# Kernel tuning notes

Hardware: AMD Instinct MI355X
Metric: run time of the kernel (lower is better)

Reference implementation:

```python
import jax, jax.numpy as jnp
import numpy as np

NUM_HEADS = 4
SPLIT_SIZE = 8  # idx == 1 -> H_sp = H, W_sp = split_size (vertical stripe windows)


def setup_inputs() -> dict:
    key = jax.random.key(0)
    k1, k2, k3 = jax.random.split(key, 3)
    temp = jax.random.normal(k1, (16, 3, 128, 64, 64), dtype=jnp.float32)
    conv_w = jax.random.normal(k2, (128, 1, 3, 3), dtype=jnp.float32) * 0.1  # depthwise LePE conv
    conv_b = jax.random.normal(k3, (128,), dtype=jnp.float32) * 0.1
    return {"temp": temp, "conv_w": conv_w, "conv_b": conv_b}


def reference(temp, conv_w, conv_b):
    B, _, C, H, W = temp.shape
    H_sp, W_sp = H, SPLIT_SIZE          # idx == 1 cross-shaped window
    # H % H_sp == 0 and W % W_sp == 0 -> F.pad amounts are zero here
    nH, nW = H // H_sp, W // W_sp
    L = H_sp * W_sp                     # tokens per window
    hd = C // NUM_HEADS
    scale = hd ** -0.5

    q, k, v = temp[:, 0], temp[:, 1], temp[:, 2]  # each [B, C, H, W]

    def im2cswin(x):
        # img2windows: B C H W -> (B*nH*nW, L, C) then split heads -> (Bw, nh, L, hd)
        x = x.reshape(B, C, nH, H_sp, nW, W_sp).transpose(0, 2, 4, 3, 5, 1)
        x = x.reshape(-1, L, NUM_HEADS, hd).transpose(0, 2, 1, 3)
        return x

    qw = im2cswin(q) * scale            # (Bw, nh, L, hd)
    kw = im2cswin(k)

    # get_rpe: window-partition v as images, depthwise 3x3 conv for LePE
    vimg = v.reshape(B, C, nH, H_sp, nW, W_sp).transpose(0, 2, 4, 1, 3, 5)
    vimg = vimg.reshape(-1, C, H_sp, W_sp)  # (Bw, C, H_sp, W_sp)
    rpe = jax.lax.conv_general_dilated(
        vimg, conv_w, window_strides=(1, 1), padding="SAME",
        dimension_numbers=("NCHW", "OIHW", "NCHW"), feature_group_count=C,
    ) + conv_b[None, :, None, None]
    rpe = rpe.reshape(-1, NUM_HEADS, hd, L).transpose(0, 1, 3, 2)  # (Bw, nh, L, hd)
    vw = vimg.reshape(-1, NUM_HEADS, hd, L).transpose(0, 1, 3, 2)

    attn = jax.nn.softmax(jnp.einsum("wnld,wnmd->wnlm", qw, kw), axis=-1)
    out = jnp.einsum("wnlm,wnmd->wnld", attn, vw) + rpe  # (Bw, nh, L, hd)

    out = out.transpose(0, 2, 1, 3).reshape(-1, L, C)    # (Bw, L, C)
    # windows2img: (Bw, L, C) -> (B, H, W, C)
    out = out.reshape(B, nH, nW, H_sp, W_sp, C).transpose(0, 1, 3, 2, 4, 5)
    out = out.reshape(B, H, W, C)
    return out.reshape(B, H * W, C)
```

## Files before the change

kernel.cpp:

```cpp
#include <hip/hip_runtime.h>

typedef __attribute__((ext_vector_type(8))) short short8;
typedef __attribute__((ext_vector_type(4))) short short4_t;
typedef __attribute__((ext_vector_type(4))) float float4_t;
typedef __attribute__((ext_vector_type(4))) int int4_t;

#define CH_STRIDE 4096
#define IMG_STRIDE 524288
#define HW 4096
#define V520 520

static __device__ __forceinline__ short f2b(float x) {
    unsigned u = __builtin_bit_cast(unsigned, x);
    u = (u + 0x7fffu + ((u >> 16) & 1u)) >> 16;
    return (short)u;
}
static __device__ __forceinline__ float bitsf(unsigned u) { return __builtin_bit_cast(float, u); }
static __device__ __forceinline__ unsigned bitsu(float f) { return __builtin_bit_cast(unsigned, f); }

__global__ __launch_bounds__(512) void cswin_fused(
    const float* __restrict__ temp, const float* __restrict__ cw,
    const float* __restrict__ cb, float* __restrict__ out)
{
    __shared__ short Kc[64 * 40];
    __shared__ short Vt[32 * V520];

    int bx = blockIdx.x;
    int nw = bx >> 6;
    int r  = bx & 63;
    int b  = r >> 2;
    int n  = r & 3;

    int t    = threadIdx.x;
    int wv   = t >> 6;
    int lane = t & 63;
    int mr   = lane & 15;
    int q    = lane >> 4;

    const float* tq = temp + (size_t)b * 3 * IMG_STRIDE + (size_t)(n * 32) * CH_STRIDE + nw * 8;
    const float* tk = tq + IMG_STRIDE;
    const float* tv = tk + IMG_STRIDE;

    int row0 = wv * 64;
    const float qscale = 0.2550348889072310f;

    short8 Qf[4];
    #pragma unroll
    for (int qt = 0; qt < 4; ++qt) {
        int l = row0 + qt * 16 + mr;
        int sp = (l >> 3) * 64 + (l & 7);
        short8 f;
        #pragma unroll
        for (int j = 0; j < 8; ++j)
            f[j] = f2b(tq[(q * 8 + j) * CH_STRIDE + sp] * qscale);
        Qf[qt] = f;
    }

    float4_t zero4 = {0.f, 0.f, 0.f, 0.f};
    float4_t acc[2][4];
    #pragma unroll
    for (int dt = 0; dt < 2; ++dt)
        #pragma unroll
        for (int qt = 0; qt < 4; ++qt)
            acc[dt][qt] = zero4;
    float lsum[4] = {0.f, 0.f, 0.f, 0.f};

    int ld  = t >> 4;
    int seg = t & 15;
    const float* tkld = tk + (size_t)ld * CH_STRIDE;
    const float* tvld = tv + (size_t)ld * CH_STRIDE;

    int lb0 = seg * 4;
    int sp0 = (lb0 >> 3) * 64 + (lb0 & 7);
    float4_t k4 = *reinterpret_cast<const float4_t*>(tkld + sp0);
    float4_t v4 = *reinterpret_cast<const float4_t*>(tvld + sp0);

    int s0lane = (q & 1) * 32 + mr;
    int s1lane = s0lane + 16;
    bool hiq = (q >= 2);

    for (int ch = 0; ch < 8; ++ch) {
        __syncthreads();
        {
            int kl = seg * 4;
            Kc[(kl + 0) * 40 + ld] = f2b(k4.x);
            Kc[(kl + 1) * 40 + ld] = f2b(k4.y);
            Kc[(kl + 2) * 40 + ld] = f2b(k4.z);
            Kc[(kl + 3) * 40 + ld] = f2b(k4.w);
            short4_t vs = { f2b(v4.x), f2b(v4.y), f2b(v4.z), f2b(v4.w) };
            *reinterpret_cast<short4_t*>(&Vt[ld * V520 + ch * 64 + kl]) = vs;
        }
        if (ch < 7) {
            int lb = (ch + 1) * 64 + seg * 4;
            int sp = (lb >> 3) * 64 + (lb & 7);
            k4 = *reinterpret_cast<const float4_t*>(tkld + sp);
            v4 = *reinterpret_cast<const float4_t*>(tvld + sp);
        }
        __syncthreads();

        #pragma unroll
        for (int g = 0; g < 2; ++g) {
            short8 KaA = *reinterpret_cast<const short8*>(&Kc[((2 * g) * 16 + mr) * 40 + q * 8]);
            short8 KaB = *reinterpret_cast<const short8*>(&Kc[((2 * g + 1) * 16 + mr) * 40 + q * 8]);
            unsigned pa0[4], pa1[4], pb0[4], pb1[4];
            #pragma unroll
            for (int qt = 0; qt < 4; ++qt) {
                float4_t sA = __builtin_amdgcn_mfma_f32_16x16x32_bf16(KaA, Qf[qt], zero4, 0, 0, 0);
                float4_t sB = __builtin_amdgcn_mfma_f32_16x16x32_bf16(KaB, Qf[qt], zero4, 0, 0, 0);
                float eA0 = __builtin_amdgcn_exp2f(sA.x), eA1 = __builtin_amdgcn_exp2f(sA.y);
                float eA2 = __builtin_amdgcn_exp2f(sA.z), eA3 = __builtin_amdgcn_exp2f(sA.w);
                float eB0 = __builtin_amdgcn_exp2f(sB.x), eB1 = __builtin_amdgcn_exp2f(sB.y);
                float eB2 = __builtin_amdgcn_exp2f(sB.z), eB3 = __builtin_amdgcn_exp2f(sB.w);
                lsum[qt] += ((eA0 + eA1) + (eA2 + eA3)) + ((eB0 + eB1) + (eB2 + eB3));
                pa0[qt] = __builtin_amdgcn_perm(bitsu(eA1), bitsu(eA0), 0x07060302u);
                pa1[qt] = __builtin_amdgcn_perm(bitsu(eA3), bitsu(eA2), 0x07060302u);
                pb0[qt] = __builtin_amdgcn_perm(bitsu(eB1), bitsu(eB0), 0x07060302u);
                pb1[qt] = __builtin_amdgcn_perm(bitsu(eB3), bitsu(eB2), 0x07060302u);
            }
            int base = ch * 64 + g * 32 + q * 8;
            short8 Va0 = *reinterpret_cast<const short8*>(&Vt[mr * V520 + base]);
            short8 Va1 = *reinterpret_cast<const short8*>(&Vt[(16 + mr) * V520 + base]);
            #pragma unroll
            for (int qt = 0; qt < 4; ++qt) {
                int x0 = __shfl((int)pa0[qt], s0lane); int y0 = __shfl((int)pb0[qt], s0lane);
                int x1 = __shfl((int)pa1[qt], s0lane); int y1 = __shfl((int)pb1[qt], s0lane);
                int x2 = __shfl((int)pa0[qt], s1lane); int y2 = __shfl((int)pb0[qt], s1lane);
                int x3 = __shfl((int)pa1[qt], s1lane); int y3 = __shfl((int)pb1[qt], s1lane);
                int4_t pi = { hiq ? y0 : x0, hiq ? y1 : x1, hiq ? y2 : x2, hiq ? y3 : x3 };
                short8 Pb = __builtin_bit_cast(short8, pi);
                acc[0][qt] = __builtin_amdgcn_mfma_f32_16x16x32_bf16(Va0, Pb, acc[0][qt], 0, 0, 0);
                acc[1][qt] = __builtin_amdgcn_mfma_f32_16x16x32_bf16(Va1, Pb, acc[1][qt], 0, 0, 0);
            }
        }
    }

    float inv[4];
    #pragma unroll
    for (int qt = 0; qt < 4; ++qt) {
        float v = lsum[qt];
        v += __shfl_xor(v, 16);
        v += __shfl_xor(v, 32);
        inv[qt] = 1.0f / v;
    }

    float* outb = out + (size_t)b * HW * 128 + nw * 8 * 128 + n * 32;
    #pragma unroll
    for (int qt = 0; qt < 4; ++qt) {
        int l = row0 + qt * 16 + mr;
        size_t basep = (size_t)((l >> 3) * 64 + (l & 7)) * 128;
        #pragma unroll
        for (int dt = 0; dt < 2; ++dt) {
            float4_t o = acc[dt][qt] * inv[qt];
            *reinterpret_cast<float4_t*>(outb + basep + dt * 16 + q * 4) = o;
        }
    }

    __syncthreads();

    int c4 = (t & 7) * 4;
    int h  = t >> 3;
    float4_t outv[8];
    #pragma unroll
    for (int cc = 0; cc < 4; ++cc) {
        int c = c4 + cc;
        float w9[9];
        #pragma unroll
        for (int i = 0; i < 9; ++i) w9[i] = cw[(n * 32 + c) * 9 + i];
        float bias = cb[n * 32 + c];
        float rv[3][8];
        #pragma unroll
        for (int rr = 0; rr < 3; ++rr) {
            int hh = h - 1 + rr;
            if (hh >= 0 && hh < 64) {
                short8 u = *reinterpret_cast<const short8*>(&Vt[c * V520 + hh * 8]);
                #pragma unroll
                for (int j = 0; j < 8; ++j)
                    rv[rr][j] = bitsf(((unsigned)(unsigned short)u[j]) << 16);
            } else {
                #pragma unroll
                for (int j = 0; j < 8; ++j) rv[rr][j] = 0.f;
            }
        }
        #pragma unroll
        for (int w = 0; w < 8; ++w) {
            float o = bias;
            #pragma unroll
            for (int rr = 0; rr < 3; ++rr) {
                if (w > 0) o += rv[rr][w - 1] * w9[rr * 3 + 0];
                o += rv[rr][w] * w9[rr * 3 + 1];
                if (w < 7) o += rv[rr][w + 1] * w9[rr * 3 + 2];
            }
            outv[w][cc] = o;
        }
    }
    #pragma unroll
    for (int w = 0; w < 8; ++w) {
        size_t off = (size_t)h * 8192 + w * 128 + c4;
        float4_t cur = *reinterpret_cast<const float4_t*>(outb + off);
        cur += outv[w];
        *reinterpret_cast<float4_t*>(outb + off) = cur;
    }
}

extern "C" void kernel_launch(void* const* d_in, const int* in_sizes, int n_in,
                              void* d_out, int out_size, void* d_ws, size_t ws_size,
                              hipStream_t stream) {
    const float* temp = (const float*)d_in[0];
    const float* cw   = (const float*)d_in[1];
    const float* cb   = (const float*)d_in[2];
    float* out = (float*)d_out;
    hipLaunchKernelGGL(cswin_fused, dim3(512), dim3(512), 0, stream, temp, cw, cb, out);
}
```

Baseline: 191.9 us.

## Double-buffer K tile in LDS and drop one barrier per chunk

Kc becomes a two-slot LDS buffer. The next chunk's K/V values are loaded before the barrier and written into the other slot after the MFMA work, so each iteration needs one __syncthreads instead of two. Global loads also change from one float4 per thread to four scalar loads strided by 16 tokens, which changes the bank pattern of the transposed LDS stores. The cost is extra LDS for the second slot and less vectorised global reads.

```diff
diff --git a/kernel.cpp b/kernel.cpp
--- a/kernel.cpp
+++ b/kernel.cpp
@@ -1,7 +1,6 @@
 #include <hip/hip_runtime.h>
 
 typedef __attribute__((ext_vector_type(8))) short short8;
-typedef __attribute__((ext_vector_type(4))) short short4_t;
 typedef __attribute__((ext_vector_type(4))) float float4_t;
 typedef __attribute__((ext_vector_type(4))) int int4_t;
 
@@ -22,7 +21,7 @@
     const float* __restrict__ temp, const float* __restrict__ cw,
     const float* __restrict__ cb, float* __restrict__ out)
 {
-    __shared__ short Kc[64 * 40];
+    __shared__ short Kc[2][64 * 40];
     __shared__ short Vt[32 * V520];
 
     int bx = blockIdx.x;
@@ -70,38 +69,42 @@
     const float* tkld = tk + (size_t)ld * CH_STRIDE;
     const float* tvld = tv + (size_t)ld * CH_STRIDE;
 
-    int lb0 = seg * 4;
-    int sp0 = (lb0 >> 3) * 64 + (lb0 & 7);
-    float4_t k4 = *reinterpret_cast<const float4_t*>(tkld + sp0);
-    float4_t v4 = *reinterpret_cast<const float4_t*>(tvld + sp0);
+    float kx[4], vx[4];
+    #pragma unroll
+    for (int i = 0; i < 4; ++i) {
+        int lb = seg + 16 * i;
+        int sp = (lb >> 3) * 64 + (lb & 7);
+        kx[i] = tkld[sp]; vx[i] = tvld[sp];
+    }
+    {
+        #pragma unroll
+        for (int i = 0; i < 4; ++i) {
+            int kl = seg + 16 * i;
+            Kc[0][kl * 40 + ld] = f2b(kx[i]);
+            Vt[ld * V520 + kl]  = f2b(vx[i]);
+        }
+    }
 
     int s0lane = (q & 1) * 32 + mr;
     int s1lane = s0lane + 16;
     bool hiq = (q >= 2);
 
     for (int ch = 0; ch < 8; ++ch) {
+        if (ch < 7) {
+            #pragma unroll
+            for (int i = 0; i < 4; ++i) {
+                int lb = (ch + 1) * 64 + seg + 16 * i;
+                int sp = (lb >> 3) * 64 + (lb & 7);
+                kx[i] = tkld[sp]; vx[i] = tvld[sp];
+            }
+        }
         __syncthreads();
-        {
-            int kl = seg * 4;
-            Kc[(kl + 0) * 40 + ld] = f2b(k4.x);
-            Kc[(kl + 1) * 40 + ld] = f2b(k4.y);
-            Kc[(kl + 2) * 40 + ld] = f2b(k4.z);
-            Kc[(kl + 3) * 40 + ld] = f2b(k4.w);
-            short4_t vs = { f2b(v4.x), f2b(v4.y), f2b(v4.z), f2b(v4.w) };
-            *reinterpret_cast<short4_t*>(&Vt[ld * V520 + ch * 64 + kl]) = vs;
-        }
-        if (ch < 7) {
-            int lb = (ch + 1) * 64 + seg * 4;
-            int sp = (lb >> 3) * 64 + (lb & 7);
-            k4 = *reinterpret_cast<const float4_t*>(tkld + sp);
-            v4 = *reinterpret_cast<const float4_t*>(tvld + sp);
-        }
-        __syncthreads();
+        const short* Kr = Kc[ch & 1];
 
         #pragma unroll
         for (int g = 0; g < 2; ++g) {
-            short8 KaA = *reinterpret_cast<const short8*>(&Kc[((2 * g) * 16 + mr) * 40 + q * 8]);
-            short8 KaB = *reinterpret_cast<const short8*>(&Kc[((2 * g + 1) * 16 + mr) * 40 + q * 8]);
+            short8 KaA = *reinterpret_cast<const short8*>(&Kr[((2 * g) * 16 + mr) * 40 + q * 8]);
+            short8 KaB = *reinterpret_cast<const short8*>(&Kr[((2 * g + 1) * 16 + mr) * 40 + q * 8]);
             unsigned pa0[4], pa1[4], pb0[4], pb1[4];
             #pragma unroll
             for (int qt = 0; qt < 4; ++qt) {
@@ -132,6 +135,16 @@
                 acc[1][qt] = __builtin_amdgcn_mfma_f32_16x16x32_bf16(Va1, Pb, acc[1][qt], 0, 0, 0);
             }
         }
+
+        if (ch < 7) {
+            short* Kw = Kc[(ch + 1) & 1];
+            #pragma unroll
+            for (int i = 0; i < 4; ++i) {
+                int kl = seg + 16 * i;
+                Kw[kl * 40 + ld] = f2b(kx[i]);
+                Vt[ld * V520 + (ch + 1) * 64 + kl] = f2b(vx[i]);
+            }
+        }
     }
 
     float inv[4];
```

New measurement: 191.1 us. About the same (-0.4%).
